# Optimization experiments

Measured on AMD Instinct MI355X. Metric: run time of the kernel, lower is better.

## Reference

```python
import jax, jax.numpy as jnp
import numpy as np

SOS = 1
EOS = 2
M = 32  # max_y_seq_len


def gru_cell(x, h, W_ih, W_hh, b_ih, b_hh):
    # torch GRUCell math: gates ordered [r, z, n]
    gi = x @ W_ih.T + b_ih          # [B, 3H]
    gh = h @ W_hh.T + b_hh          # [B, 3H]
    i_r, i_z, i_n = jnp.split(gi, 3, axis=-1)
    h_r, h_z, h_n = jnp.split(gh, 3, axis=-1)
    r = jax.nn.sigmoid(i_r + h_r)
    z = jax.nn.sigmoid(i_z + h_z)
    n = jnp.tanh(i_n + r * h_n)
    return (1.0 - z) * n + z * h


def setup_inputs() -> dict:
    key = jax.random.key(0)
    ks = jax.random.split(key, 12)
    B, H, V = 256, 512, 16000
    s = 0.05  # keep GRU pre-activations in a sane range
    return {
        "sem_f": jax.random.normal(ks[0], (B, H), jnp.float32),
        "emb": jax.random.normal(ks[1], (V, H), jnp.float32) * 0.01,
        "W_ih0": jax.random.normal(ks[2], (3 * H, H), jnp.float32) * s,
        "W_hh0": jax.random.normal(ks[3], (3 * H, H), jnp.float32) * s,
        "b_ih0": jax.random.normal(ks[4], (3 * H,), jnp.float32) * s,
        "b_hh0": jax.random.normal(ks[5], (3 * H,), jnp.float32) * s,
        "W_ih1": jax.random.normal(ks[6], (3 * H, H), jnp.float32) * s,
        "W_hh1": jax.random.normal(ks[7], (3 * H, H), jnp.float32) * s,
        "b_ih1": jax.random.normal(ks[8], (3 * H,), jnp.float32) * s,
        "b_hh1": jax.random.normal(ks[9], (3 * H,), jnp.float32) * s,
        "fc_W": jax.random.normal(ks[10], (V, H), jnp.float32) * s,
        "fc_b": jax.random.normal(ks[11], (V,), jnp.float32) * s,
    }


def reference(sem_f, emb, W_ih0, W_hh0, b_ih0, b_hh0,
              W_ih1, W_hh1, b_ih1, b_hh1, fc_W, fc_b):
    B = sem_f.shape[0]
    # hidden = sem_f repeated for each GRU layer
    h0 = sem_f
    h1 = sem_f
    inputs = jnp.full((B,), SOS, dtype=jnp.int32)
    finished = jnp.zeros((B,), dtype=bool)

    def step(carry, _):
        inputs, h0, h1, finished = carry
        unf = ~finished                         # rows still active this step
        x = emb[inputs]                         # [B, H]
        h0n = gru_cell(x, h0, W_ih0, W_hh0, b_ih0, b_hh0)
        h1n = gru_cell(h0n, h1, W_ih1, W_hh1, b_ih1, b_hh1)
        out = h1n @ fc_W.T + fc_b               # [B, V]
        dec = jnp.argmax(out, axis=1).astype(jnp.int32)
        # emulate unf_idxs advanced-indexing writes: finished rows keep -1 / 0
        decoded_t = jnp.where(unf, dec, -1)
        logits_t = jnp.where(unf[:, None], out, 0.0)
        new_finished = finished | (unf & (dec == EOS))
        # pruned (finished) rows freeze hidden and inputs
        h0 = jnp.where(unf[:, None], h0n, h0)
        h1 = jnp.where(unf[:, None], h1n, h1)
        inputs = jnp.where(unf, dec, inputs)
        return (inputs, h0, h1, new_finished), (decoded_t, logits_t)

    _, (decoded, logits) = jax.lax.scan(step, (inputs, h0, h1, finished),
                                        None, length=M)
    decoded = decoded.T                          # [B, M]
    logits = jnp.transpose(logits, (1, 0, 2))    # [B, M, V]
    mask = decoded != -1
    return decoded, logits, mask
```

## Files before the change

### kernel.cpp

```cpp
#include <hip/hip_runtime.h>
#include <math.h>

#define B_   256
#define H_   512
#define V_   16000
#define M_   32
#define SOS_ 1
#define EOS_ 2
#define INV_SCALE (1.0f/2048.0f)

typedef _Float16 half_t;
typedef _Float16 f16x8 __attribute__((ext_vector_type(8)));
typedef _Float16 f16x4 __attribute__((ext_vector_type(4)));
typedef float    f32x4 __attribute__((ext_vector_type(4)));

__device__ __forceinline__ void split_f32(float x, half_t& a, half_t& b) {
    a = (half_t)x;
    b = (half_t)((x - (float)a) * 2048.0f);
}

__global__ __launch_bounds__(256)
void split_weights(const float* __restrict__ src, half_t* __restrict__ hi,
                   half_t* __restrict__ lo, int n4)
{
    const int i = blockIdx.x * 256 + threadIdx.x;
    if (i >= n4) return;
    const float4 v = ((const float4*)src)[i];
    f16x4 a, b;
    half_t t0, t1;
    split_f32(v.x, t0, t1); a[0] = t0; b[0] = t1;
    split_f32(v.y, t0, t1); a[1] = t0; b[1] = t1;
    split_f32(v.z, t0, t1); a[2] = t0; b[2] = t1;
    split_f32(v.w, t0, t1); a[3] = t0; b[3] = t1;
    ((f16x4*)hi)[i] = a;
    ((f16x4*)lo)[i] = b;
}

__global__ __launch_bounds__(256)
void init_kernel(const float* __restrict__ sem_f, const float* __restrict__ emb,
                 float* __restrict__ h0, float* __restrict__ h1,
                 half_t* __restrict__ h0a, half_t* __restrict__ h0b,
                 half_t* __restrict__ h1a, half_t* __restrict__ h1b,
                 half_t* __restrict__ xa,  half_t* __restrict__ xb,
                 int* __restrict__ inputs, int* __restrict__ finished)
{
    const int i = blockIdx.x * 256 + threadIdx.x;
    if (i < B_ * H_) {
        const float v = sem_f[i];
        h0[i] = v; h1[i] = v;
        half_t a, b; split_f32(v, a, b);
        h0a[i] = a; h0b[i] = b;
        h1a[i] = a; h1b[i] = b;
        const int j = i & (H_ - 1);
        const float xv = emb[SOS_ * H_ + j];
        half_t c, d; split_f32(xv, c, d);
        xa[i] = c; xb[i] = d;
    }
    if (i < B_) { inputs[i] = SOS_; finished[i] = 0; }
}

__global__ __launch_bounds__(256)
void gru_gemm_mfma(const half_t* __restrict__ Aia, const half_t* __restrict__ Aib,
                   const half_t* __restrict__ Aha, const half_t* __restrict__ Ahb,
                   const half_t* __restrict__ Wia, const half_t* __restrict__ Wib,
                   const half_t* __restrict__ Wha, const half_t* __restrict__ Whb,
                   const float* __restrict__ b_ih, const float* __restrict__ b_hh,
                   float* __restrict__ PRE)
{
    const int ct = blockIdx.x;
    const int rt = blockIdx.y;
    const bool is_ih = (ct < 12);
    const int wrow0 = (is_ih ? ct : ct - 12) * 128;
    const int row0  = rt * 32;
    const float*  bias = is_ih ? b_ih : b_hh;
    const half_t* Aa   = is_ih ? Aia : Aha;
    const half_t* Ab   = is_ih ? Aib : Ahb;
    const half_t* W0   = is_ih ? Wia : Wha;
    const half_t* W1   = is_ih ? Wib : Whb;

    __shared__ half_t W0s[128][40];
    __shared__ half_t W1s[128][40];

    const int tid  = threadIdx.x;
    const int w    = tid >> 6;
    const int lane = tid & 63;
    const int ll   = lane & 15;
    const int lg   = lane >> 4;

    const int sc = tid >> 1;
    const int sk = (tid & 1) * 16;
    const half_t* wp0 = W0 + (size_t)(wrow0 + sc) * H_ + sk;
    const half_t* wp1 = W1 + (size_t)(wrow0 + sc) * H_ + sk;

    f32x4 accM[2][2] = {};
    f32x4 accC[2][2] = {};

    for (int k0 = 0; k0 < H_; k0 += 32) {
        const f16x8 s0 = *(const f16x8*)(wp0 + k0);
        const f16x8 s1 = *(const f16x8*)(wp0 + k0 + 8);
        const f16x8 s2 = *(const f16x8*)(wp1 + k0);
        const f16x8 s3 = *(const f16x8*)(wp1 + k0 + 8);
        __syncthreads();
        *(f16x8*)&W0s[sc][sk]     = s0;
        *(f16x8*)&W0s[sc][sk + 8] = s1;
        *(f16x8*)&W1s[sc][sk]     = s2;
        *(f16x8*)&W1s[sc][sk + 8] = s3;
        __syncthreads();

        f16x8 a0[2], a1[2];
#pragma unroll
        for (int rf = 0; rf < 2; ++rf) {
            const size_t off = ((size_t)(row0 + 16*rf + ll) << 9) + k0 + (lg << 3);
            a0[rf] = *(const f16x8*)(Aa + off);
            a1[rf] = *(const f16x8*)(Ab + off);
        }
#pragma unroll
        for (int cf = 0; cf < 2; ++cf) {
            const int c = 32*w + 16*cf + ll;
            const f16x8 b0 = *(const f16x8*)&W0s[c][lg << 3];
            const f16x8 b1 = *(const f16x8*)&W1s[c][lg << 3];
#pragma unroll
            for (int rf = 0; rf < 2; ++rf) {
                accM[rf][cf] = __builtin_amdgcn_mfma_f32_16x16x32_f16(a0[rf], b0, accM[rf][cf], 0,0,0);
                accC[rf][cf] = __builtin_amdgcn_mfma_f32_16x16x32_f16(a0[rf], b1, accC[rf][cf], 0,0,0);
                accC[rf][cf] = __builtin_amdgcn_mfma_f32_16x16x32_f16(a1[rf], b0, accC[rf][cf], 0,0,0);
            }
        }
    }

#pragma unroll
    for (int cf = 0; cf < 2; ++cf) {
        const int cl = 32*w + 16*cf + ll;
        const float bv = bias[wrow0 + cl];
        const int c = ct * 128 + cl;
#pragma unroll
        for (int rf = 0; rf < 2; ++rf) {
#pragma unroll
            for (int r = 0; r < 4; ++r) {
                const int row = row0 + 16*rf + lg*4 + r;
                PRE[(size_t)row * 3072 + c] = accM[rf][cf][r] + accC[rf][cf][r] * INV_SCALE + bv;
            }
        }
    }
}

__global__ __launch_bounds__(256)
void gate_kernel(const float* __restrict__ PRE,
                 float* __restrict__ h,
                 half_t* __restrict__ ha, half_t* __restrict__ hb,
                 const int* __restrict__ finished)
{
    const int idx = blockIdx.x * 256 + threadIdx.x;
    const int b = idx >> 9;
    const int j = idx & 511;
    if (finished[b]) return;
    const float* p = PRE + (size_t)b * 3072;
    const float ir = p[j],        iz = p[512 + j],  in_ = p[1024 + j];
    const float hr = p[1536 + j], hz = p[2048 + j], hn  = p[2560 + j];
    const float r = 1.0f / (1.0f + expf(-(ir + hr)));
    const float z = 1.0f / (1.0f + expf(-(iz + hz)));
    const float n = tanhf(in_ + r * hn);
    const float hv = (1.0f - z) * n + z * h[idx];
    h[idx] = hv;
    half_t a, bb; split_f32(hv, a, bb);
    ha[idx] = a; hb[idx] = bb;
}

__global__ __launch_bounds__(256)
void fc_gemm_mfma(const half_t* __restrict__ Aa, const half_t* __restrict__ Ab,
                  const half_t* __restrict__ W0, const half_t* __restrict__ W1,
                  const float* __restrict__ fcb,
                  const int* __restrict__ finished,
                  float* __restrict__ logits,
                  float* __restrict__ pmax, int* __restrict__ pidx, int t)
{
    const int ct = blockIdx.x;
    const int rt = blockIdx.y;
    const int col0 = ct * 128;
    const int row0 = rt * 64;

    __shared__ half_t W0s[128][40];
    __shared__ half_t W1s[128][40];
    __shared__ float  pmS[64][2];
    __shared__ int    piS[64][2];

    const int tid  = threadIdx.x;
    const int wv   = tid >> 6;
    const int wr   = wv >> 1, wc = wv & 1;
    const int lane = tid & 63;
    const int ll   = lane & 15, lg = lane >> 4;

    const int sc = tid >> 1;
    const int sk = (tid & 1) * 16;
    const half_t* wp0 = W0 + (size_t)(col0 + sc) * H_ + sk;
    const half_t* wp1 = W1 + (size_t)(col0 + sc) * H_ + sk;

    f32x4 accM[2][4] = {};
    f32x4 accC[2][4] = {};

    for (int k0 = 0; k0 < H_; k0 += 32) {
        const f16x8 s0 = *(const f16x8*)(wp0 + k0);
        const f16x8 s1 = *(const f16x8*)(wp0 + k0 + 8);
        const f16x8 s2 = *(const f16x8*)(wp1 + k0);
        const f16x8 s3 = *(const f16x8*)(wp1 + k0 + 8);
        __syncthreads();
        *(f16x8*)&W0s[sc][sk]     = s0;
        *(f16x8*)&W0s[sc][sk + 8] = s1;
        *(f16x8*)&W1s[sc][sk]     = s2;
        *(f16x8*)&W1s[sc][sk + 8] = s3;
        __syncthreads();

        f16x8 a0[2], a1[2];
#pragma unroll
        for (int rf = 0; rf < 2; ++rf) {
            const size_t off = ((size_t)(row0 + 32*wr + 16*rf + ll) << 9) + k0 + (lg << 3);
            a0[rf] = *(const f16x8*)(Aa + off);
            a1[rf] = *(const f16x8*)(Ab + off);
        }
#pragma unroll
        for (int cf = 0; cf < 4; ++cf) {
            const int c = 64*wc + 16*cf + ll;
            const f16x8 b0 = *(const f16x8*)&W0s[c][lg << 3];
            const f16x8 b1 = *(const f16x8*)&W1s[c][lg << 3];
#pragma unroll
            for (int rf = 0; rf < 2; ++rf) {
                accM[rf][cf] = __builtin_amdgcn_mfma_f32_16x16x32_f16(a0[rf], b0, accM[rf][cf], 0,0,0);
                accC[rf][cf] = __builtin_amdgcn_mfma_f32_16x16x32_f16(a0[rf], b1, accC[rf][cf], 0,0,0);
                accC[rf][cf] = __builtin_amdgcn_mfma_f32_16x16x32_f16(a1[rf], b0, accC[rf][cf], 0,0,0);
            }
        }
    }

    int fin[2][4];
#pragma unroll
    for (int rf = 0; rf < 2; ++rf)
#pragma unroll
        for (int r = 0; r < 4; ++r)
            fin[rf][r] = finished[row0 + 32*wr + 16*rf + lg*4 + r];

    float bvv[2][4];
    int   bii[2][4];
#pragma unroll
    for (int rf = 0; rf < 2; ++rf)
#pragma unroll
        for (int r = 0; r < 4; ++r) { bvv[rf][r] = -INFINITY; bii[rf][r] = 0x7fffffff; }

#pragma unroll
    for (int cf = 0; cf < 4; ++cf) {
        const int col = col0 + 64*wc + 16*cf + ll;
        const float bv = fcb[col];
#pragma unroll
        for (int rf = 0; rf < 2; ++rf) {
#pragma unroll
            for (int r = 0; r < 4; ++r) {
                const int row = row0 + 32*wr + 16*rf + lg*4 + r;
                const float raw = accM[rf][cf][r] + accC[rf][cf][r] * INV_SCALE + bv;
                logits[((size_t)row * M_ + t) * V_ + col] = fin[rf][r] ? 0.0f : raw;
                if (raw > bvv[rf][r]) { bvv[rf][r] = raw; bii[rf][r] = col; }
            }
        }
    }

#pragma unroll
    for (int rf = 0; rf < 2; ++rf) {
#pragma unroll
        for (int r = 0; r < 4; ++r) {
            float v = bvv[rf][r]; int ix = bii[rf][r];
#pragma unroll
            for (int m = 1; m < 16; m <<= 1) {
                const float ov = __shfl_xor(v, m);
                const int   oi = __shfl_xor(ix, m);
                if (ov > v || (ov == v && oi < ix)) { v = ov; ix = oi; }
            }
            if (ll == 0) {
                const int lr = 32*wr + 16*rf + lg*4 + r;
                pmS[lr][wc] = v; piS[lr][wc] = ix;
            }
        }
    }
    __syncthreads();
    if (tid < 64) {
        float v = pmS[tid][0]; int ix = piS[tid][0];
        const float v2 = pmS[tid][1]; const int i2 = piS[tid][1];
        if (v2 > v || (v2 == v && i2 < ix)) { v = v2; ix = i2; }
        pmax[(row0 + tid) * 128 + ct] = v;
        pidx[(row0 + tid) * 128 + ct] = ix;
    }
}

__global__ __launch_bounds__(128)
void finalize_kernel(const float* __restrict__ pmax, const int* __restrict__ pidx,
                     const float* __restrict__ emb,
                     int* __restrict__ inputs, int* __restrict__ finished,
                     float* __restrict__ decoded_out, float* __restrict__ mask_out,
                     half_t* __restrict__ xa, half_t* __restrict__ xb, int t)
{
    const int b = blockIdx.x;
    const int tid = threadIdx.x;
    __shared__ float sv[128];
    __shared__ int   si[128];
    float v = -INFINITY; int ix = 0x7fffffff;
    if (tid < 125) { v = pmax[b * 128 + tid]; ix = pidx[b * 128 + tid]; }
    sv[tid] = v; si[tid] = ix;
    __syncthreads();
    for (int s = 64; s > 0; s >>= 1) {
        if (tid < s) {
            const float v2 = sv[tid + s]; const int i2 = si[tid + s];
            if (v2 > sv[tid] || (v2 == sv[tid] && i2 < si[tid])) { sv[tid] = v2; si[tid] = i2; }
        }
        __syncthreads();
    }
    __shared__ int s_tok;
    if (tid == 0) {
        const int fin = finished[b];
        const int dec = si[0];
        decoded_out[b * M_ + t] = fin ? -1.0f : (float)dec;
        mask_out   [b * M_ + t] = fin ? 0.0f : 1.0f;
        int tok;
        if (!fin) { inputs[b] = dec; if (dec == EOS_) finished[b] = 1; tok = dec; }
        else tok = inputs[b];
        s_tok = tok;
    }
    __syncthreads();
    const int tok = s_tok;
    for (int j = tid; j < H_; j += 128) {
        const float v2 = emb[(size_t)tok * H_ + j];
        half_t a, bb; split_f32(v2, a, bb);
        xa[b * H_ + j] = a; xb[b * H_ + j] = bb;
    }
}

extern "C" void kernel_launch(void* const* d_in, const int* in_sizes, int n_in,
                              void* d_out, int out_size, void* d_ws, size_t ws_size,
                              hipStream_t stream)
{
    const float* sem_f = (const float*)d_in[0];
    const float* emb   = (const float*)d_in[1];
    const float* W_ih0 = (const float*)d_in[2];
    const float* W_hh0 = (const float*)d_in[3];
    const float* b_ih0 = (const float*)d_in[4];
    const float* b_hh0 = (const float*)d_in[5];
    const float* W_ih1 = (const float*)d_in[6];
    const float* W_hh1 = (const float*)d_in[7];
    const float* b_ih1 = (const float*)d_in[8];
    const float* b_hh1 = (const float*)d_in[9];
    const float* fc_W  = (const float*)d_in[10];
    const float* fc_b  = (const float*)d_in[11];

    float* out = (float*)d_out;
    float* decoded_out = out;
    float* logits_out  = out + (size_t)B_ * M_;
    float* mask_out    = out + (size_t)B_ * M_ + (size_t)B_ * M_ * V_;

    float*  ws  = (float*)d_ws;
    float*  PRE = ws;
    float*  h0  = ws + 786432;
    float*  h1  = ws + 917504;
    half_t* h0a = (half_t*)(ws + 1048576);
    half_t* h0b = (half_t*)(ws + 1114112);
    half_t* h1a = (half_t*)(ws + 1179648);
    half_t* h1b = (half_t*)(ws + 1245184);
    half_t* xa  = (half_t*)(ws + 1310720);
    half_t* xb  = (half_t*)(ws + 1376256);
    float*  pmax = ws + 1441792;
    int*    pidx = (int*)(ws + 1474560);
    int*    inputs   = (int*)(ws + 1507328);
    int*    finished = (int*)(ws + 1507584);
    half_t* wi0a = (half_t*)(ws + 1507840);
    half_t* wi0b = (half_t*)(ws + 1901056);
    half_t* wh0a = (half_t*)(ws + 2294272);
    half_t* wh0b = (half_t*)(ws + 2687488);
    half_t* wi1a = (half_t*)(ws + 3080704);
    half_t* wi1b = (half_t*)(ws + 3473920);
    half_t* wh1a = (half_t*)(ws + 3867136);
    half_t* wh1b = (half_t*)(ws + 4260352);
    half_t* fca  = (half_t*)(ws + 4653568);
    half_t* fcbp = (half_t*)(ws + 8749568);

    const int nGru4 = (1536 * 512) / 4;
    const int nFc4  = (V_ * H_) / 4;
    split_weights<<<(nGru4 + 255) / 256, 256, 0, stream>>>(W_ih0, wi0a, wi0b, nGru4);
    split_weights<<<(nGru4 + 255) / 256, 256, 0, stream>>>(W_hh0, wh0a, wh0b, nGru4);
    split_weights<<<(nGru4 + 255) / 256, 256, 0, stream>>>(W_ih1, wi1a, wi1b, nGru4);
    split_weights<<<(nGru4 + 255) / 256, 256, 0, stream>>>(W_hh1, wh1a, wh1b, nGru4);
    split_weights<<<(nFc4 + 255) / 256, 256, 0, stream>>>(fc_W, fca, fcbp, nFc4);

    init_kernel<<<(B_ * H_ + 255) / 256, 256, 0, stream>>>(
        sem_f, emb, h0, h1, h0a, h0b, h1a, h1b, xa, xb, inputs, finished);

    const dim3 gruGrid(24, 8);
    const dim3 fcGrid(125, 4);

    for (int t = 0; t < M_; ++t) {
        gru_gemm_mfma<<<gruGrid, 256, 0, stream>>>(
            xa, xb, h0a, h0b, wi0a, wi0b, wh0a, wh0b, b_ih0, b_hh0, PRE);
        gate_kernel<<<(B_ * H_) / 256, 256, 0, stream>>>(PRE, h0, h0a, h0b, finished);
        gru_gemm_mfma<<<gruGrid, 256, 0, stream>>>(
            h0a, h0b, h1a, h1b, wi1a, wi1b, wh1a, wh1b, b_ih1, b_hh1, PRE);
        gate_kernel<<<(B_ * H_) / 256, 256, 0, stream>>>(PRE, h1, h1a, h1b, finished);
        fc_gemm_mfma<<<fcGrid, 256, 0, stream>>>(
            h1a, h1b, fca, fcbp, fc_b, finished, logits_out, pmax, pidx, t);
        finalize_kernel<<<B_, 128, 0, stream>>>(
            pmax, pidx, emb, inputs, finished, decoded_out, mask_out, xa, xb, t);
    }
}
```

Measured before the change: 2.979 ms.

## Load GRU GEMM operands directly from global memory with 64x64 tiles

The GRU gate GEMM no longer stages the weight tile through shared memory with two barriers per k-step. Each wave now reads its A and B fragments straight from global memory. Block tiles change from 32x128 to 64x64, each wave owns a 32x32 sub-tile, and the 1D grid stays at 192 blocks. This removes LDS traffic and synchronisation, at the cost of relying on L1/L2 for operand reuse and issuing more redundant global loads.

```diff
diff --git a/kernel.cpp b/kernel.cpp
--- a/kernel.cpp
+++ b/kernel.cpp
@@ -20,14 +20,13 @@
 }
 
 __global__ __launch_bounds__(256)
-void split_weights(const float* __restrict__ src, half_t* __restrict__ hi,
-                   half_t* __restrict__ lo, int n4)
+void split_weights_k(const float* __restrict__ src, half_t* __restrict__ hi,
+                     half_t* __restrict__ lo, int n4)
 {
     const int i = blockIdx.x * 256 + threadIdx.x;
     if (i >= n4) return;
     const float4 v = ((const float4*)src)[i];
-    f16x4 a, b;
-    half_t t0, t1;
+    f16x4 a, b; half_t t0, t1;
     split_f32(v.x, t0, t1); a[0] = t0; b[0] = t1;
     split_f32(v.y, t0, t1); a[1] = t0; b[1] = t1;
     split_f32(v.z, t0, t1); a[2] = t0; b[2] = t1;
@@ -59,88 +58,71 @@
     if (i < B_) { inputs[i] = SOS_; finished[i] = 0; }
 }
 
-__global__ __launch_bounds__(256)
-void gru_gemm_mfma(const half_t* __restrict__ Aia, const half_t* __restrict__ Aib,
-                   const half_t* __restrict__ Aha, const half_t* __restrict__ Ahb,
-                   const half_t* __restrict__ Wia, const half_t* __restrict__ Wib,
-                   const half_t* __restrict__ Wha, const half_t* __restrict__ Whb,
-                   const float* __restrict__ b_ih, const float* __restrict__ b_hh,
-                   float* __restrict__ PRE)
-{
-    const int ct = blockIdx.x;
-    const int rt = blockIdx.y;
-    const bool is_ih = (ct < 12);
-    const int wrow0 = (is_ih ? ct : ct - 12) * 128;
-    const int row0  = rt * 32;
+__global__ __launch_bounds__(256, 2)
+void gru_bf_k(const half_t* __restrict__ Aia, const half_t* __restrict__ Aib,
+              const half_t* __restrict__ Aha, const half_t* __restrict__ Ahb,
+              const half_t* __restrict__ Wia, const half_t* __restrict__ Wib,
+              const half_t* __restrict__ Wha, const half_t* __restrict__ Whb,
+              const float* __restrict__ b_ih, const float* __restrict__ b_hh,
+              float* __restrict__ PRE)
+{
+    const int bidx = blockIdx.x;
+    const int ct = bidx % 48;
+    const int rt = bidx / 48;
+    const bool is_ih = (ct < 24);
+    const int wrow0 = (is_ih ? ct : ct - 24) * 64;
+    const int row0  = rt * 64;
     const float*  bias = is_ih ? b_ih : b_hh;
-    const half_t* Aa   = is_ih ? Aia : Aha;
-    const half_t* Ab   = is_ih ? Aib : Ahb;
-    const half_t* W0   = is_ih ? Wia : Wha;
-    const half_t* W1   = is_ih ? Wib : Whb;
-
-    __shared__ half_t W0s[128][40];
-    __shared__ half_t W1s[128][40];
+    const half_t* Aa = is_ih ? Aia : Aha;
+    const half_t* Ab = is_ih ? Aib : Ahb;
+    const half_t* W0 = is_ih ? Wia : Wha;
+    const half_t* W1 = is_ih ? Wib : Whb;
 
     const int tid  = threadIdx.x;
-    const int w    = tid >> 6;
+    const int wv   = tid >> 6;
+    const int wr   = wv >> 1, wc = wv & 1;
     const int lane = tid & 63;
-    const int ll   = lane & 15;
-    const int lg   = lane >> 4;
-
-    const int sc = tid >> 1;
-    const int sk = (tid & 1) * 16;
-    const half_t* wp0 = W0 + (size_t)(wrow0 + sc) * H_ + sk;
-    const half_t* wp1 = W1 + (size_t)(wrow0 + sc) * H_ + sk;
+    const int ll   = lane & 15, lg = lane >> 4;
 
     f32x4 accM[2][2] = {};
     f32x4 accC[2][2] = {};
 
+    const size_t aoff0 = ((size_t)(row0 + 32*wr + ll) << 9) + (lg << 3);
+    const size_t boff0 = ((size_t)(wrow0 + 32*wc + ll) << 9) + (lg << 3);
+
+#pragma unroll 2
     for (int k0 = 0; k0 < H_; k0 += 32) {
-        const f16x8 s0 = *(const f16x8*)(wp0 + k0);
-        const f16x8 s1 = *(const f16x8*)(wp0 + k0 + 8);
-        const f16x8 s2 = *(const f16x8*)(wp1 + k0);
-        const f16x8 s3 = *(const f16x8*)(wp1 + k0 + 8);
-        __syncthreads();
-        *(f16x8*)&W0s[sc][sk]     = s0;
-        *(f16x8*)&W0s[sc][sk + 8] = s1;
-        *(f16x8*)&W1s[sc][sk]     = s2;
-        *(f16x8*)&W1s[sc][sk + 8] = s3;
-        __syncthreads();
-
-        f16x8 a0[2], a1[2];
-#pragma unroll
-        for (int rf = 0; rf < 2; ++rf) {
-            const size_t off = ((size_t)(row0 + 16*rf + ll) << 9) + k0 + (lg << 3);
-            a0[rf] = *(const f16x8*)(Aa + off);
-            a1[rf] = *(const f16x8*)(Ab + off);
-        }
-#pragma unroll
-        for (int cf = 0; cf < 2; ++cf) {
-            const int c = 32*w + 16*cf + ll;
-            const f16x8 b0 = *(const f16x8*)&W0s[c][lg << 3];
-            const f16x8 b1 = *(const f16x8*)&W1s[c][lg << 3];
+        f16x8 a0[2], a1[2], b0[2], b1[2];
+        a0[0] = *(const f16x8*)(Aa + aoff0 + k0);
+        a0[1] = *(const f16x8*)(Aa + aoff0 + 8192 + k0);
+        a1[0] = *(const f16x8*)(Ab + aoff0 + k0);
+        a1[1] = *(const f16x8*)(Ab + aoff0 + 8192 + k0);
+        b0[0] = *(const f16x8*)(W0 + boff0 + k0);
+        b0[1] = *(const f16x8*)(W0 + boff0 + 8192 + k0);
+        b1[0] = *(const f16x8*)(W1 + boff0 + k0);
+        b1[1] = *(const f16x8*)(W1 + boff0 + 8192 + k0);
+#pragma unroll
+        for (int cf = 0; cf < 2; ++cf)
 #pragma unroll
             for (int rf = 0; rf < 2; ++rf) {
-                accM[rf][cf] = __builtin_amdgcn_mfma_f32_16x16x32_f16(a0[rf], b0, accM[rf][cf], 0,0,0);
-                accC[rf][cf] = __builtin_amdgcn_mfma_f32_16x16x32_f16(a0[rf], b1, accC[rf][cf], 0,0,0);
-                accC[rf][cf] = __builtin_amdgcn_mfma_f32_16x16x32_f16(a1[rf], b0, accC[rf][cf], 0,0,0);
-            }
-        }
+                accM[rf][cf] = __builtin_amdgcn_mfma_f32_16x16x32_f16(a0[rf], b0[cf], accM[rf][cf], 0,0,0);
+                accC[rf][cf] = __builtin_amdgcn_mfma_f32_16x16x32_f16(a0[rf], b1[cf], accC[rf][cf], 0,0,0);
+                accC[rf][cf] = __builtin_amdgcn_mfma_f32_16x16x32_f16(a1[rf], b0[cf], accC[rf][cf], 0,0,0);
+            }
     }
 
 #pragma unroll
     for (int cf = 0; cf < 2; ++cf) {
-        const int cl = 32*w + 16*cf + ll;
+        const int cl = 32*wc + 16*cf + ll;
         const float bv = bias[wrow0 + cl];
-        const int c = ct * 128 + cl;
-#pragma unroll
-        for (int rf = 0; rf < 2; ++rf) {
+        const int c = ct * 64 + cl;
+#pragma unroll
+        for (int rf = 0; rf < 2; ++rf)
 #pragma unroll
             for (int r = 0; r < 4; ++r) {
-                const int row = row0 + 16*rf + lg*4 + r;
+                const int row = row0 + 32*wr + 16*rf + lg*4 + r;
                 PRE[(size_t)row * 3072 + c] = accM[rf][cf][r] + accC[rf][cf][r] * INV_SCALE + bv;
             }
-        }
     }
 }
 
@@ -379,23 +361,22 @@
 
     const int nGru4 = (1536 * 512) / 4;
     const int nFc4  = (V_ * H_) / 4;
-    split_weights<<<(nGru4 + 255) / 256, 256, 0, stream>>>(W_ih0, wi0a, wi0b, nGru4);
-    split_weights<<<(nGru4 + 255) / 256, 256, 0, stream>>>(W_hh0, wh0a, wh0b, nGru4);
-    split_weights<<<(nGru4 + 255) / 256, 256, 0, stream>>>(W_ih1, wi1a, wi1b, nGru4);
-    split_weights<<<(nGru4 + 255) / 256, 256, 0, stream>>>(W_hh1, wh1a, wh1b, nGru4);
-    split_weights<<<(nFc4 + 255) / 256, 256, 0, stream>>>(fc_W, fca, fcbp, nFc4);
+    split_weights_k<<<(nGru4 + 255) / 256, 256, 0, stream>>>(W_ih0, wi0a, wi0b, nGru4);
+    split_weights_k<<<(nGru4 + 255) / 256, 256, 0, stream>>>(W_hh0, wh0a, wh0b, nGru4);
+    split_weights_k<<<(nGru4 + 255) / 256, 256, 0, stream>>>(W_ih1, wi1a, wi1b, nGru4);
+    split_weights_k<<<(nGru4 + 255) / 256, 256, 0, stream>>>(W_hh1, wh1a, wh1b, nGru4);
+    split_weights_k<<<(nFc4 + 255) / 256, 256, 0, stream>>>(fc_W, fca, fcbp, nFc4);
 
     init_kernel<<<(B_ * H_ + 255) / 256, 256, 0, stream>>>(
         sem_f, emb, h0, h1, h0a, h0b, h1a, h1b, xa, xb, inputs, finished);
 
-    const dim3 gruGrid(24, 8);
     const dim3 fcGrid(125, 4);
 
     for (int t = 0; t < M_; ++t) {
-        gru_gemm_mfma<<<gruGrid, 256, 0, stream>>>(
+        gru_bf_k<<<192, 256, 0, stream>>>(
             xa, xb, h0a, h0b, wi0a, wi0b, wh0a, wh0b, b_ih0, b_hh0, PRE);
         gate_kernel<<<(B_ * H_) / 256, 256, 0, stream>>>(PRE, h0, h0a, h0b, finished);
-        gru_gemm_mfma<<<gruGrid, 256, 0, stream>>>(
+        gru_bf_k<<<192, 256, 0, stream>>>(
             h0a, h0b, h1a, h1b, wi1a, wi1b, wh1a, wh1b, b_ih1, b_hh1, PRE);
         gate_kernel<<<(B_ * H_) / 256, 256, 0, stream>>>(PRE, h1, h1a, h1b, finished);
         fc_gemm_mfma<<<fcGrid, 256, 0, stream>>>(
```

After: 2.980 ms. About the same (+0.1%).
